# Optimization experiments

Hardware: AMD Instinct MI355X
Metric: run time of the kernel (lower is better)

Reference implementation:

```python
import jax, jax.numpy as jnp
import numpy as np

B, N, F_IN, F_OUT, T, E = 2, 50000, 2, 32, 12, 800000


def _uniform(k, shape, scale):
    return jax.random.uniform(k, shape, jnp.float32, -scale, scale)


def setup_inputs() -> dict:
    key = jax.random.key(0)
    ks = jax.random.split(key, 18)
    inp = {
        "X": jax.random.normal(ks[0], (B, N, F_IN, T), dtype=jnp.float32),
        "edge_index": jax.random.randint(ks[1], (2, E), 0, N, dtype=jnp.int64),
        "edge_weight": jax.random.uniform(ks[2], (E,), dtype=jnp.float32),
    }
    # GCNConv weights [F_IN, F_OUT] (glorot) + bias, for gates z, r, h
    g = float(np.sqrt(6.0 / (F_IN + F_OUT)))
    inp["Wz"] = _uniform(ks[3], (F_IN, F_OUT), g); inp["bz"] = jnp.zeros((F_OUT,), jnp.float32)
    inp["Wr"] = _uniform(ks[4], (F_IN, F_OUT), g); inp["br"] = jnp.zeros((F_OUT,), jnp.float32)
    inp["Wh"] = _uniform(ks[5], (F_IN, F_OUT), g); inp["bh"] = jnp.zeros((F_OUT,), jnp.float32)
    # Linear(2*F_OUT -> F_OUT) per gate (stored as [2*F_OUT, F_OUT] for x @ W)
    l = float(np.sqrt(1.0 / (2 * F_OUT)))
    inp["Lz_w"] = _uniform(ks[6], (2 * F_OUT, F_OUT), l); inp["Lz_b"] = _uniform(ks[7], (F_OUT,), l)
    inp["Lr_w"] = _uniform(ks[8], (2 * F_OUT, F_OUT), l); inp["Lr_b"] = _uniform(ks[9], (F_OUT,), l)
    inp["Lh_w"] = _uniform(ks[10], (2 * F_OUT, F_OUT), l); inp["Lh_b"] = _uniform(ks[11], (F_OUT,), l)
    # attention logits over periods, init uniform(0,1)
    inp["attention"] = jax.random.uniform(ks[12], (T,), dtype=jnp.float32)
    return inp


def _a3tgcn(X, edge_index, edge_weight, Wz, bz, Wr, br, Wh, bh,
            Lz_w, Lz_b, Lr_w, Lr_b, Lh_w, Lh_b, attention):
    n = X.shape[1]
    loop = jnp.arange(n)
    row = jnp.concatenate([edge_index[0], loop])  # sources (+ self loops)
    col = jnp.concatenate([edge_index[1], loop])  # targets
    w = jnp.concatenate([edge_weight, jnp.ones((n,), X.dtype)])
    deg = jax.ops.segment_sum(w, col, num_segments=n)
    dinv = jnp.where(deg > 0, jax.lax.rsqrt(deg), 0.0)
    norm = dinv[row] * w * dinv[col]  # [E+N] sym-normalized coeffs

    def gcn(x, W, b):
        xw = jnp.einsum('bnf,fo->bno', x, W)                # [B,N,O]
        msg = xw[:, row, :] * norm[None, :, None]           # [B,E+N,O]
        agg = jax.vmap(lambda m: jax.ops.segment_sum(m, col, num_segments=n))(msg)
        return agg + b

    probs = jax.nn.softmax(attention)
    H0 = jnp.zeros((X.shape[0], n, Wz.shape[1]), X.dtype)

    def step(carry, inputs):
        H, acc = carry
        Xt, p = inputs  # Xt: [B,N,F_IN]
        Z = jax.nn.sigmoid(jnp.concatenate([gcn(Xt, Wz, bz), H], -1) @ Lz_w + Lz_b)
        R = jax.nn.sigmoid(jnp.concatenate([gcn(Xt, Wr, br), H], -1) @ Lr_w + Lr_b)
        Ht = jnp.tanh(jnp.concatenate([gcn(Xt, Wh, bh), H * R], -1) @ Lh_w + Lh_b)
        Hn = Z * H + (1.0 - Z) * Ht
        return (Hn, acc + p * Hn), None

    xs = jnp.moveaxis(X, -1, 0)  # [T,B,N,F_IN]
    (_, H_accum), _ = jax.lax.scan(step, (H0, H0), (xs, probs))
    return H_accum


def reference(X, edge_index, edge_weight, Wz, bz, Wr, br, Wh, bh,
              Lz_w, Lz_b, Lr_w, Lr_b, Lh_w, Lh_b, attention):
    return _a3tgcn(X, edge_index, edge_weight, Wz, bz, Wr, br, Wh, bh,
                   Lz_w, Lz_b, Lr_w, Lr_b, Lh_w, Lh_b, attention)
```

## Files before the change

kernel.cpp:

```cpp
#include <hip/hip_runtime.h>

#define NN 50000
#define EE 800000
#define TT 12
#define BB 2

#define OFF_AX   50048
#define OFF_P    2450048
#define OFF_CNT  2454144
#define OFF_OFF  2504192
#define OFF_CUR  2554240
#define OFF_BSUM 2604288
#define NB_SCAN  98
#define NNODES   (BB * NN)
#define NW       4
#define NBLK_REC 6250

__device__ __forceinline__ float fsig(float x) {
    x = fminf(fmaxf(x, -30.f), 30.f);
    return __builtin_amdgcn_rcpf(1.f + __expf(-x));
}
__device__ __forceinline__ float ftanh(float x) {
    x = fminf(fmaxf(x, -15.f), 15.f);
    float e = __expf(-2.f * x);
    return (1.f - e) * __builtin_amdgcn_rcpf(1.f + e);
}

__global__ void k_zero(int* __restrict__ cnt) {
    int i = blockIdx.x * 256 + threadIdx.x;
    if (i < NN) cnt[i] = 0;
}

__global__ void k_count(const int* __restrict__ idx, int* __restrict__ cnt) {
    int e = blockIdx.x * 256 + threadIdx.x;
    if (e < EE) atomicAdd(&cnt[idx[EE + e]], 1);
}

__global__ void k_scanA(const int* __restrict__ cnt, int* __restrict__ off,
                        int* __restrict__ bsum) {
    __shared__ int sm[512];
    int i = blockIdx.x * 512 + threadIdx.x;
    int v = (i < NN) ? cnt[i] : 0;
    sm[threadIdx.x] = v;
    __syncthreads();
#pragma unroll
    for (int d = 1; d < 512; d <<= 1) {
        int t = (threadIdx.x >= d) ? sm[threadIdx.x - d] : 0;
        __syncthreads();
        sm[threadIdx.x] += t;
        __syncthreads();
    }
    if (i < NN) off[i] = sm[threadIdx.x] - v;
    if (threadIdx.x == 511) bsum[blockIdx.x] = sm[511];
}

__global__ void k_scanB(int* __restrict__ bsum) {
    __shared__ int sm[128];
    int tid = threadIdx.x;
    int v = (tid < NB_SCAN) ? bsum[tid] : 0;
    sm[tid] = v;
    __syncthreads();
#pragma unroll
    for (int d = 1; d < 128; d <<= 1) {
        int t = (tid >= d) ? sm[tid - d] : 0;
        __syncthreads();
        sm[tid] += t;
        __syncthreads();
    }
    if (tid < NB_SCAN) bsum[tid] = sm[tid] - v;
}

__global__ void k_scanC(int* __restrict__ off, const int* __restrict__ bsum,
                        int* __restrict__ cur) {
    int i = blockIdx.x * 256 + threadIdx.x;
    if (i < NN) {
        int o = off[i] + bsum[i >> 9];
        off[i] = o;
        cur[i] = o;
    }
}

__global__ void k_fill(const int* __restrict__ idx, const float* __restrict__ w,
                       int* __restrict__ cur, int* __restrict__ esrc,
                       float* __restrict__ ewgt) {
    int e = blockIdx.x * 256 + threadIdx.x;
    if (e >= EE) return;
    int c = idx[EE + e];
    int s = atomicAdd(&cur[c], 1);
    esrc[s] = idx[e];
    ewgt[s] = w[e];
}

__global__ void k_degdinv(const int* __restrict__ off, const int* __restrict__ cnt,
                          const float* __restrict__ ewgt, float* __restrict__ dinv) {
    int n = blockIdx.x * 256 + threadIdx.x;
    if (n >= NN) return;
    int s0 = off[n], c = cnt[n];
    float d = 1.f;
    for (int q = 0; q < c; q++) d += ewgt[s0 + q];
    dinv[n] = rsqrtf(d);
}

__global__ __launch_bounds__(256) void k_gather(const float* __restrict__ X,
                                                const float* __restrict__ dinv,
                                                const int* __restrict__ esrc,
                                                const float* __restrict__ ewgt,
                                                const int* __restrict__ off,
                                                const int* __restrict__ cnt,
                                                float* __restrict__ AX) {
    int tid = blockIdx.x * 256 + threadIdx.x;
    if (tid >= NNODES) return;
    int b = tid / NN;
    int n = tid - b * NN;
    float di = dinv[n];
    const float* Xb = X + (size_t)b * NN * 24;

    float xf[24], acc[24];
    {
        const float4* xs = (const float4*)(Xb + (size_t)n * 24);
        float s = di * di;
#pragma unroll
        for (int q = 0; q < 6; q++) {
            float4 v = xs[q];
            xf[4 * q] = v.x; xf[4 * q + 1] = v.y; xf[4 * q + 2] = v.z; xf[4 * q + 3] = v.w;
        }
#pragma unroll
        for (int t = 0; t < TT; t++) {
            acc[2 * t] = s * xf[t];
            acc[2 * t + 1] = s * xf[12 + t];
        }
    }
    int s0 = off[n], c = cnt[n];
    for (int q = 0; q < c; q++) {
        int r = esrc[s0 + q];
        float nrm = dinv[r] * ewgt[s0 + q] * di;
        const float4* xr = (const float4*)(Xb + (size_t)r * 24);
#pragma unroll
        for (int p = 0; p < 6; p++) {
            float4 v = xr[p];
            xf[4 * p] = v.x; xf[4 * p + 1] = v.y; xf[4 * p + 2] = v.z; xf[4 * p + 3] = v.w;
        }
#pragma unroll
        for (int t = 0; t < TT; t++) {
            acc[2 * t] = fmaf(nrm, xf[t], acc[2 * t]);
            acc[2 * t + 1] = fmaf(nrm, xf[12 + t], acc[2 * t + 1]);
        }
    }
    float4* o = (float4*)(AX + (size_t)tid * 24);
#pragma unroll
    for (int q = 0; q < 6; q++)
        o[q] = make_float4(acc[4 * q], acc[4 * q + 1], acc[4 * q + 2], acc[4 * q + 3]);
}

__global__ void k_fold(const float* __restrict__ Wz, const float* __restrict__ bz,
                       const float* __restrict__ Lwz, const float* __restrict__ Lbz,
                       const float* __restrict__ Wr, const float* __restrict__ br,
                       const float* __restrict__ Lwr, const float* __restrict__ Lbr,
                       const float* __restrict__ Wh, const float* __restrict__ bh,
                       const float* __restrict__ Lwh, const float* __restrict__ Lbh,
                       const float* __restrict__ att, float* __restrict__ P) {
    int tid = threadIdx.x;
    if (tid < 96) {
        int g = tid >> 5, j = tid & 31;
        const float* W  = g == 0 ? Wz  : (g == 1 ? Wr  : Wh);
        const float* b  = g == 0 ? bz  : (g == 1 ? br  : bh);
        const float* Lw = g == 0 ? Lwz : (g == 1 ? Lwr : Lwh);
        const float* Lb = g == 0 ? Lbz : (g == 1 ? Lbr : Lbh);
        float* out = P + g * 1120;
        float w0 = 0.f, w1 = 0.f, c = 0.f;
        for (int k = 0; k < 32; k++) {
            float lw = Lw[k * 32 + j];
            w0 += W[k] * lw;
            w1 += W[32 + k] * lw;
            c  += b[k] * lw;
        }
        out[j] = w0;
        out[32 + j] = w1;
        out[64 + j] = c + Lb[j];
        for (int k = 0; k < 32; k++) out[96 + k * 32 + j] = Lw[(32 + k) * 32 + j];
    } else if (tid == 96) {
        float m = -1e30f;
        for (int t = 0; t < TT; t++) m = fmaxf(m, att[t]);
        float s = 0.f;
        float e[TT];
        for (int t = 0; t < TT; t++) { e[t] = __expf(att[t] - m); s += e[t]; }
        for (int t = 0; t < TT; t++) P[3360 + t] = e[t] / s;
    }
}

__global__ __launch_bounds__(256) void k_recur(const float* __restrict__ AX,
                                               const float* __restrict__ P,
                                               float* __restrict__ out) {
    __shared__ __align__(16) float Hs[NW][32];
    __shared__ __align__(16) float rHs[NW][32];
    __shared__ __align__(16) float AXs[NW][24];
    const int lane = threadIdx.x & 63;
    const int w = threadIdx.x >> 6;
    const int j = lane & 31;
    const int h = lane >> 5;
    const int k0 = h * 16;
    const int gwave = blockIdx.x * NW + w;

    float LBz[16], LBr[16], LBh[16];
    float wz0 = P[j],        wz1 = P[32 + j],        cz = P[64 + j];
    float wr0 = P[1120 + j], wr1 = P[1120 + 32 + j], cr = P[1120 + 64 + j];
    float wh0 = P[2240 + j], wh1 = P[2240 + 32 + j], ch = P[2240 + 64 + j];
#pragma unroll
    for (int k = 0; k < 16; k++) {
        LBz[k] = P[96 + (k0 + k) * 32 + j];
        LBr[k] = P[1120 + 96 + (k0 + k) * 32 + j];
        LBh[k] = P[2240 + 96 + (k0 + k) * 32 + j];
    }

#pragma unroll 1
    for (int node = gwave; node < NNODES; node += NBLK_REC * NW) {
        if (lane < 24) AXs[w][lane] = AX[(size_t)node * 24 + lane];

        float2 a = *(const float2*)&AXs[w][0];
        float z = fsig(fmaf(a.x, wz0, fmaf(a.y, wz1, cz)));
        float th = ftanh(fmaf(a.x, wh0, fmaf(a.y, wh1, ch)));
        float H = (1.f - z) * th;
        float acc = P[3360] * H;
        if (lane < 32) Hs[w][j] = H;

#pragma unroll 1
        for (int t = 1; t < TT; t++) {
            a = *(const float2*)&AXs[w][2 * t];
            float hb[16];
#pragma unroll
            for (int i = 0; i < 4; i++) {
                float4 v = *(const float4*)&Hs[w][k0 + 4 * i];
                hb[4 * i] = v.x; hb[4 * i + 1] = v.y;
                hb[4 * i + 2] = v.z; hb[4 * i + 3] = v.w;
            }
            float sr;
            {
                float s0 = 0.f, s1 = 0.f, s2 = 0.f, s3 = 0.f;
#pragma unroll
                for (int k = 0; k < 16; k += 4) {
                    s0 = fmaf(hb[k],     LBr[k],     s0);
                    s1 = fmaf(hb[k + 1], LBr[k + 1], s1);
                    s2 = fmaf(hb[k + 2], LBr[k + 2], s2);
                    s3 = fmaf(hb[k + 3], LBr[k + 3], s3);
                }
                sr = (s0 + s1) + (s2 + s3);
            }
            sr += __shfl_xor(sr, 32, 64);
            float rH = fsig(fmaf(a.x, wr0, fmaf(a.y, wr1, cr)) + sr) * H;
            if (lane < 32) rHs[w][j] = rH;
            float sz;
            {
                float s0 = 0.f, s1 = 0.f, s2 = 0.f, s3 = 0.f;
#pragma unroll
                for (int k = 0; k < 16; k += 4) {
                    s0 = fmaf(hb[k],     LBz[k],     s0);
                    s1 = fmaf(hb[k + 1], LBz[k + 1], s1);
                    s2 = fmaf(hb[k + 2], LBz[k + 2], s2);
                    s3 = fmaf(hb[k + 3], LBz[k + 3], s3);
                }
                sz = (s0 + s1) + (s2 + s3);
            }
            sz += __shfl_xor(sz, 32, 64);
            z = fsig(fmaf(a.x, wz0, fmaf(a.y, wz1, cz)) + sz);
            float rb[16];
#pragma unroll
            for (int i = 0; i < 4; i++) {
                float4 v = *(const float4*)&rHs[w][k0 + 4 * i];
                rb[4 * i] = v.x; rb[4 * i + 1] = v.y;
                rb[4 * i + 2] = v.z; rb[4 * i + 3] = v.w;
            }
            float sh;
            {
                float s0 = 0.f, s1 = 0.f, s2 = 0.f, s3 = 0.f;
#pragma unroll
                for (int k = 0; k < 16; k += 4) {
                    s0 = fmaf(rb[k],     LBh[k],     s0);
                    s1 = fmaf(rb[k + 1], LBh[k + 1], s1);
                    s2 = fmaf(rb[k + 2], LBh[k + 2], s2);
                    s3 = fmaf(rb[k + 3], LBh[k + 3], s3);
                }
                sh = (s0 + s1) + (s2 + s3);
            }
            sh += __shfl_xor(sh, 32, 64);
            th = ftanh(fmaf(a.x, wh0, fmaf(a.y, wh1, ch)) + sh);
            float Hn = fmaf(z, H - th, th);
            H = Hn;
            acc = fmaf(P[3360 + t], Hn, acc);
            if (lane < 32 && t < TT - 1) Hs[w][j] = Hn;
        }
        if (lane < 32) out[(size_t)node * 32 + j] = acc;
    }
}

extern "C" void kernel_launch(void* const* d_in, const int* in_sizes, int n_in,
                              void* d_out, int out_size, void* d_ws, size_t ws_size,
                              hipStream_t stream) {
    const float* X   = (const float*)d_in[0];
    const int*   idx = (const int*)d_in[1];
    const float* ew  = (const float*)d_in[2];
    const float* Wz  = (const float*)d_in[3];
    const float* bz  = (const float*)d_in[4];
    const float* Wr  = (const float*)d_in[5];
    const float* br  = (const float*)d_in[6];
    const float* Wh  = (const float*)d_in[7];
    const float* bh  = (const float*)d_in[8];
    const float* Lwz = (const float*)d_in[9];
    const float* Lbz = (const float*)d_in[10];
    const float* Lwr = (const float*)d_in[11];
    const float* Lbr = (const float*)d_in[12];
    const float* Lwh = (const float*)d_in[13];
    const float* Lbh = (const float*)d_in[14];
    const float* att = (const float*)d_in[15];

    float* ws   = (float*)d_ws;
    float* dinv = ws;
    float* AX   = ws + OFF_AX;
    float* P    = ws + OFF_P;
    int*   cnt  = (int*)ws + OFF_CNT;
    int*   off  = (int*)ws + OFF_OFF;
    int*   cur  = (int*)ws + OFF_CUR;
    int*   bsum = (int*)ws + OFF_BSUM;
    float* out  = (float*)d_out;
    int*   esrc = (int*)d_out;
    float* ewgt = (float*)d_out + EE;

    hipLaunchKernelGGL(k_zero, dim3((NN + 255) / 256), dim3(256), 0, stream, cnt);
    hipLaunchKernelGGL(k_count, dim3((EE + 255) / 256), dim3(256), 0, stream, idx, cnt);
    hipLaunchKernelGGL(k_scanA, dim3(NB_SCAN), dim3(512), 0, stream, cnt, off, bsum);
    hipLaunchKernelGGL(k_scanB, dim3(1), dim3(128), 0, stream, bsum);
    hipLaunchKernelGGL(k_scanC, dim3((NN + 255) / 256), dim3(256), 0, stream, off, bsum, cur);
    hipLaunchKernelGGL(k_fill, dim3((EE + 255) / 256), dim3(256), 0, stream, idx, ew, cur, esrc, ewgt);
    hipLaunchKernelGGL(k_degdinv, dim3((NN + 255) / 256), dim3(256), 0, stream, off, cnt, ewgt, dinv);
    hipLaunchKernelGGL(k_gather, dim3((NNODES + 255) / 256), dim3(256), 0, stream,
                       X, dinv, esrc, ewgt, off, cnt, AX);
    hipLaunchKernelGGL(k_fold, dim3(1), dim3(128), 0, stream,
                       Wz, bz, Lwz, Lbz, Wr, br, Lwr, Lbr, Wh, bh, Lwh, Lbh, att, P);
    hipLaunchKernelGGL(k_recur, dim3(NBLK_REC), dim3(256), 0, stream, AX, P, out);
}
```

Measured before the change: 335.2 us.

## Pack edge source and weight, resize gather and recurrence blocks, memset counts

Edge source index and weight are now stored interleaved as int2, so the CSR fill, degree and gather kernels read both with a single 8-byte load instead of two separate arrays. The gather kernel moves to 64-thread blocks and the recurrence kernel to 512-thread blocks with 8 waves each. The zeroing kernel is replaced by hipMemsetAsync. Together these aim to cut scattered memory transactions and launch overhead, but the new block sizes change occupancy and scheduling granularity.

```diff
diff --git a/kernel.cpp b/kernel.cpp
--- a/kernel.cpp
+++ b/kernel.cpp
@@ -13,8 +13,8 @@
 #define OFF_BSUM 2604288
 #define NB_SCAN  98
 #define NNODES   (BB * NN)
-#define NW       4
-#define NBLK_REC 6250
+#define NW       8
+#define NBLK_REC 3125
 
 __device__ __forceinline__ float fsig(float x) {
     x = fminf(fmaxf(x, -30.f), 30.f);
@@ -24,11 +24,6 @@
     x = fminf(fmaxf(x, -15.f), 15.f);
     float e = __expf(-2.f * x);
     return (1.f - e) * __builtin_amdgcn_rcpf(1.f + e);
-}
-
-__global__ void k_zero(int* __restrict__ cnt) {
-    int i = blockIdx.x * 256 + threadIdx.x;
-    if (i < NN) cnt[i] = 0;
 }
 
 __global__ void k_count(const int* __restrict__ idx, int* __restrict__ cnt) {
@@ -81,34 +76,31 @@
 }
 
 __global__ void k_fill(const int* __restrict__ idx, const float* __restrict__ w,
-                       int* __restrict__ cur, int* __restrict__ esrc,
-                       float* __restrict__ ewgt) {
+                       int* __restrict__ cur, int2* __restrict__ epack) {
     int e = blockIdx.x * 256 + threadIdx.x;
     if (e >= EE) return;
     int c = idx[EE + e];
     int s = atomicAdd(&cur[c], 1);
-    esrc[s] = idx[e];
-    ewgt[s] = w[e];
+    epack[s] = make_int2(idx[e], __float_as_int(w[e]));
 }
 
 __global__ void k_degdinv(const int* __restrict__ off, const int* __restrict__ cnt,
-                          const float* __restrict__ ewgt, float* __restrict__ dinv) {
+                          const int2* __restrict__ epack, float* __restrict__ dinv) {
     int n = blockIdx.x * 256 + threadIdx.x;
     if (n >= NN) return;
     int s0 = off[n], c = cnt[n];
     float d = 1.f;
-    for (int q = 0; q < c; q++) d += ewgt[s0 + q];
+    for (int q = 0; q < c; q++) d += __int_as_float(epack[s0 + q].y);
     dinv[n] = rsqrtf(d);
 }
 
-__global__ __launch_bounds__(256) void k_gather(const float* __restrict__ X,
-                                                const float* __restrict__ dinv,
-                                                const int* __restrict__ esrc,
-                                                const float* __restrict__ ewgt,
-                                                const int* __restrict__ off,
-                                                const int* __restrict__ cnt,
-                                                float* __restrict__ AX) {
-    int tid = blockIdx.x * 256 + threadIdx.x;
+__global__ __launch_bounds__(64) void k_gather(const float* __restrict__ X,
+                                               const float* __restrict__ dinv,
+                                               const int2* __restrict__ epack,
+                                               const int* __restrict__ off,
+                                               const int* __restrict__ cnt,
+                                               float* __restrict__ AX) {
+    int tid = blockIdx.x * 64 + threadIdx.x;
     if (tid >= NNODES) return;
     int b = tid / NN;
     int n = tid - b * NN;
@@ -132,8 +124,9 @@
     }
     int s0 = off[n], c = cnt[n];
     for (int q = 0; q < c; q++) {
-        int r = esrc[s0 + q];
-        float nrm = dinv[r] * ewgt[s0 + q] * di;
+        int2 ep = epack[s0 + q];
+        int r = ep.x;
+        float nrm = dinv[r] * __int_as_float(ep.y) * di;
         const float4* xr = (const float4*)(Xb + (size_t)r * 24);
 #pragma unroll
         for (int p = 0; p < 6; p++) {
@@ -188,7 +181,7 @@
     }
 }
 
-__global__ __launch_bounds__(256) void k_recur(const float* __restrict__ AX,
+__global__ __launch_bounds__(512) void k_recur(const float* __restrict__ AX,
                                                const float* __restrict__ P,
                                                float* __restrict__ out) {
     __shared__ __align__(16) float Hs[NW][32];
@@ -321,19 +314,18 @@
     int*   cur  = (int*)ws + OFF_CUR;
     int*   bsum = (int*)ws + OFF_BSUM;
     float* out  = (float*)d_out;
-    int*   esrc = (int*)d_out;
-    float* ewgt = (float*)d_out + EE;
-
-    hipLaunchKernelGGL(k_zero, dim3((NN + 255) / 256), dim3(256), 0, stream, cnt);
+    int2*  epack = (int2*)d_out;
+
+    hipMemsetAsync(cnt, 0, NN * sizeof(int), stream);
     hipLaunchKernelGGL(k_count, dim3((EE + 255) / 256), dim3(256), 0, stream, idx, cnt);
     hipLaunchKernelGGL(k_scanA, dim3(NB_SCAN), dim3(512), 0, stream, cnt, off, bsum);
     hipLaunchKernelGGL(k_scanB, dim3(1), dim3(128), 0, stream, bsum);
     hipLaunchKernelGGL(k_scanC, dim3((NN + 255) / 256), dim3(256), 0, stream, off, bsum, cur);
-    hipLaunchKernelGGL(k_fill, dim3((EE + 255) / 256), dim3(256), 0, stream, idx, ew, cur, esrc, ewgt);
-    hipLaunchKernelGGL(k_degdinv, dim3((NN + 255) / 256), dim3(256), 0, stream, off, cnt, ewgt, dinv);
-    hipLaunchKernelGGL(k_gather, dim3((NNODES + 255) / 256), dim3(256), 0, stream,
-                       X, dinv, esrc, ewgt, off, cnt, AX);
+    hipLaunchKernelGGL(k_fill, dim3((EE + 255) / 256), dim3(256), 0, stream, idx, ew, cur, epack);
+    hipLaunchKernelGGL(k_degdinv, dim3((NN + 255) / 256), dim3(256), 0, stream, off, cnt, epack, dinv);
+    hipLaunchKernelGGL(k_gather, dim3((NNODES + 63) / 64), dim3(64), 0, stream,
+                       X, dinv, epack, off, cnt, AX);
     hipLaunchKernelGGL(k_fold, dim3(1), dim3(128), 0, stream,
                        Wz, bz, Lwz, Lbz, Wr, br, Lwr, Lbr, Wh, bh, Lwh, Lbh, att, P);
-    hipLaunchKernelGGL(k_recur, dim3(NBLK_REC), dim3(256), 0, stream, AX, P, out);
-}
+    hipLaunchKernelGGL(k_recur, dim3(NBLK_REC), dim3(512), 0, stream, AX, P, out);
+}
```

Measured after the change: 331.4 us. No clear change (-1.1%).
